# Performance work log

Measured on AMD Instinct MI355X. Metric: run time of the kernel, lower is better.

## Reference

```python
import jax, jax.numpy as jnp
import numpy as np

B, S, Lb, C, CP, H = 64, 4, 64, 32, 16, 4
LN_EPS = 1e-5


def layer_norm(x, g, b):
    mu = jnp.mean(x, axis=-1, keepdims=True)
    var = jnp.mean(jnp.square(x - mu), axis=-1, keepdims=True)
    return (x - mu) * jax.lax.rsqrt(var + LN_EPS) * g + b


def mha(x, w_in, b_in, w_out, b_out, h):
    # torch nn.MultiheadAttention, batch_first, self-attention
    Bx, L, Cx = x.shape
    d = Cx // h
    qkv = x @ w_in.T + b_in                      # (Bx, L, 3C)
    q, k, v = jnp.split(qkv, 3, axis=-1)
    sp = lambda t: t.reshape(Bx, L, h, d).transpose(0, 2, 1, 3)  # (Bx,h,L,d)
    q, k, v = sp(q), sp(k), sp(v)
    scale = 1.0 / jnp.sqrt(jnp.asarray(d, x.dtype))
    attn = jax.nn.softmax(jnp.einsum('bhid,bhjd->bhij', q, k) * scale, axis=-1)
    o = jnp.einsum('bhij,bhjd->bhid', attn, v).transpose(0, 2, 1, 3).reshape(Bx, L, Cx)
    return o @ w_out.T + b_out


def setup_inputs() -> dict:
    key = jax.random.key(0)
    ks = jax.random.split(key, 20)
    g = lambda i, shape, s=0.05: (jax.random.normal(ks[i], shape, dtype=jnp.float32) * s)
    inp = {
        'chip_ctcf': jax.random.normal(ks[0], (B, Lb), dtype=jnp.float32),
        'chip_hac':  jax.random.normal(ks[1], (B, Lb), dtype=jnp.float32),
        'chip_me1':  jax.random.normal(ks[2], (B, Lb), dtype=jnp.float32),
        'chip_me3':  jax.random.normal(ks[3], (B, Lb), dtype=jnp.float32),
        'embed_w': g(4, (C, 1)), 'embed_b': g(5, (C,)),
        'pos_embed': g(6, (1, 1, Lb, C), 0.02),
        'row_in_w': g(7, (3 * C, C)), 'row_in_b': g(8, (3 * C,)),
        'row_out_w': g(9, (C, C)), 'row_out_b': g(10, (C,)),
        'row_ln_g': jnp.ones((C,), jnp.float32), 'row_ln_b': jnp.zeros((C,), jnp.float32),
        'col_in_w': g(11, (3 * C, C)), 'col_in_b': g(12, (3 * C,)),
        'col_out_w': g(13, (C, C)), 'col_out_b': g(14, (C,)),
        'col_ln_g': jnp.ones((C,), jnp.float32), 'col_ln_b': jnp.zeros((C,), jnp.float32),
        'proj_w': g(15, (CP, C * C)), 'proj_b': g(16, (CP,)),
        'pln_g': jnp.ones((CP,), jnp.float32), 'pln_b': jnp.zeros((CP,), jnp.float32),
    }
    return inp


def reference(chip_ctcf, chip_hac, chip_me1, chip_me3,
              embed_w, embed_b, pos_embed,
              row_in_w, row_in_b, row_out_w, row_out_b, row_ln_g, row_ln_b,
              col_in_w, col_in_b, col_out_w, col_out_b, col_ln_g, col_ln_b,
              proj_w, proj_b, pln_g, pln_b):
    Bv = chip_ctcf.shape[0]
    signals = jnp.stack([chip_ctcf, chip_hac, chip_me1, chip_me3], axis=1)  # (B,4,64)
    # Linear(1, C): scalar embed
    msa = signals[..., None] * embed_w[:, 0] + embed_b                      # (B,4,64,C)
    msa = msa + pos_embed
    # row attention over the 64 bins, per track
    x = msa.reshape(Bv * S, Lb, C)
    x = layer_norm(x + mha(x, row_in_w, row_in_b, row_out_w, row_out_b, H), row_ln_g, row_ln_b)
    msa = x.reshape(Bv, S, Lb, C)
    # column attention over the 4 tracks, per bin
    x = msa.transpose(0, 2, 1, 3).reshape(Bv * Lb, S, C)
    x = layer_norm(x + mha(x, col_in_w, col_in_b, col_out_w, col_out_b, H), col_ln_g, col_ln_b)
    msa = x.reshape(Bv, Lb, S, C).transpose(0, 2, 1, 3)                     # (B,4,64,C)
    # outer product of the track-mean (as written in the torch source)
    m = jnp.mean(msa, axis=1)                                               # (B,64,C)
    pair = jnp.einsum('bic,bjd->bijcd', m, m).reshape(Bv, Lb, Lb, C * C)    # (B,64,64,1024)
    nrm = jnp.sqrt(jnp.sum(jnp.square(pair), axis=-1, keepdims=True))
    pair = pair / jnp.maximum(nrm, 1e-6)                                    # F.normalize eps=1e-6
    feat = pair @ proj_w.T + proj_b                                         # (B,64,64,CP)
    feat = layer_norm(feat, pln_g, pln_b)
    feat = feat * jax.nn.sigmoid(feat)                                      # SiLU
    return feat.transpose(0, 3, 1, 2)                                       # (B,CP,64,64)
```

## Files before the change

kernel.cpp:

```cpp
#include <hip/hip_runtime.h>

#define LN_EPS 1e-5f

__device__ __forceinline__ float dot8(float4 a0, float4 a1, float4 b0, float4 b1) {
    return a0.x * b0.x + a0.y * b0.y + a0.z * b0.z + a0.w * b0.w +
           a1.x * b1.x + a1.y * b1.y + a1.z * b1.z + a1.w * b1.w;
}

__global__ __launch_bounds__(512, 4) void k_row(
    const float* __restrict__ ctcf, const float* __restrict__ hac,
    const float* __restrict__ me1,  const float* __restrict__ me3,
    const float* __restrict__ ew,   const float* __restrict__ eb,
    const float* __restrict__ pe,
    const float* __restrict__ w_in, const float* __restrict__ b_in,
    const float* __restrict__ w_out,const float* __restrict__ b_out,
    const float* __restrict__ ln_g, const float* __restrict__ ln_b,
    float* __restrict__ msaR)
{
    __shared__ float sx[64][33];
    __shared__ float sqkv[64 * 100];
    __shared__ float so[32][33];

    const int blk = blockIdx.x;
    const int qh  = blk & 1;
    const int s   = (blk >> 1) & 3;
    const int b   = blk >> 3;
    const int qbase = qh * 32;
    const int tid = threadIdx.x;

    const float* chip = (s == 0) ? ctcf : (s == 1) ? hac : (s == 2) ? me1 : me3;

    const int l  = tid & 63;
    const int cg = __builtin_amdgcn_readfirstlane(tid >> 6);

    float xr[32];
    {
        const float cv = chip[b * 64 + l];
        const float4* pe4 = (const float4*)&pe[l * 32];
        const float4* ew4 = (const float4*)ew;
        const float4* eb4 = (const float4*)eb;
#pragma unroll
        for (int c4 = 0; c4 < 8; ++c4) {
            float4 pv = pe4[c4], e = ew4[c4], bb = eb4[c4];
            xr[c4 * 4 + 0] = cv * e.x + bb.x + pv.x;
            xr[c4 * 4 + 1] = cv * e.y + bb.y + pv.y;
            xr[c4 * 4 + 2] = cv * e.z + bb.z + pv.z;
            xr[c4 * 4 + 3] = cv * e.w + bb.w + pv.w;
        }
    }
    if (cg == 0) {
#pragma unroll
        for (int c = 0; c < 32; ++c) sx[l][c] = xr[c];
    }

#pragma unroll
    for (int i = 0; i < 12; ++i) {
        const int cc = i * 8 + cg;
        const float4* wr4 = (const float4*)&w_in[cc * 32];
        float acc = b_in[cc];
#pragma unroll
        for (int c4 = 0; c4 < 8; ++c4) {
            float4 wv = wr4[c4];
            acc += xr[c4 * 4 + 0] * wv.x + xr[c4 * 4 + 1] * wv.y +
                   xr[c4 * 4 + 2] * wv.z + xr[c4 * 4 + 3] * wv.w;
        }
        sqkv[l * 100 + cc] = acc;
    }
    __syncthreads();

    {
        const int h  = tid >> 7;
        const int q  = (tid >> 2) & 31;
        const int kc = tid & 3;
        const int lq = qbase + q;
        const float4* qp = (const float4*)&sqkv[lq * 100 + h * 8];
        float4 q0 = qp[0], q1 = qp[1];
        const float scale = 0.35355339059327373f;

        float sc[16];
#pragma unroll
        for (int jj = 0; jj < 16; ++jj) {
            const int j = kc * 16 + ((jj + kc) & 15);
            const float4* kp = (const float4*)&sqkv[j * 100 + 32 + h * 8];
            sc[jj] = dot8(q0, q1, kp[0], kp[1]) * scale;
        }
        float m0 = fmaxf(fmaxf(fmaxf(sc[0], sc[1]),  fmaxf(sc[2], sc[3])),
                         fmaxf(fmaxf(sc[4], sc[5]),  fmaxf(sc[6], sc[7])));
        float m1 = fmaxf(fmaxf(fmaxf(sc[8], sc[9]),  fmaxf(sc[10], sc[11])),
                         fmaxf(fmaxf(sc[12], sc[13]), fmaxf(sc[14], sc[15])));
        float mx = fmaxf(m0, m1);
        mx = fmaxf(mx, __shfl_xor(mx, 1, 64));
        mx = fmaxf(mx, __shfl_xor(mx, 2, 64));

        float den = 0.f, a[8];
#pragma unroll
        for (int dd = 0; dd < 8; ++dd) a[dd] = 0.f;
#pragma unroll
        for (int jj = 0; jj < 16; ++jj) {
            const int j = kc * 16 + ((jj + kc) & 15);
            float w = __expf(sc[jj] - mx);
            den += w;
            const float4* vp = (const float4*)&sqkv[j * 100 + 64 + h * 8];
            float4 v0 = vp[0], v1 = vp[1];
            a[0] += w * v0.x;  a[1] += w * v0.y;
            a[2] += w * v0.z;  a[3] += w * v0.w;
            a[4] += w * v1.x;  a[5] += w * v1.y;
            a[6] += w * v1.z;  a[7] += w * v1.w;
        }
#pragma unroll
        for (int off = 1; off <= 2; off <<= 1) {
            den += __shfl_xor(den, off, 64);
#pragma unroll
            for (int dd = 0; dd < 8; ++dd) a[dd] += __shfl_xor(a[dd], off, 64);
        }
        float inv = 1.f / den;
        float r0, r1;
        if      (kc == 0) { r0 = a[0]; r1 = a[1]; }
        else if (kc == 1) { r0 = a[2]; r1 = a[3]; }
        else if (kc == 2) { r0 = a[4]; r1 = a[5]; }
        else              { r0 = a[6]; r1 = a[7]; }
        so[q][h * 8 + kc * 2 + 0] = r0 * inv;
        so[q][h * 8 + kc * 2 + 1] = r1 * inv;
    }
    __syncthreads();

    {
        const int lq2 = tid & 31;
        const int cB  = tid >> 5;
        float orow[32];
#pragma unroll
        for (int k = 0; k < 32; ++k) orow[k] = so[lq2][k];
#pragma unroll
        for (int i = 0; i < 2; ++i) {
            int c = cB + i * 16;
            const float4* wr4 = (const float4*)&w_out[c * 32];
            float acc = b_out[c] + sx[qbase + lq2][c];
#pragma unroll
            for (int k4 = 0; k4 < 8; ++k4) {
                float4 wv = wr4[k4];
                acc += orow[k4 * 4 + 0] * wv.x + orow[k4 * 4 + 1] * wv.y +
                       orow[k4 * 4 + 2] * wv.z + orow[k4 * 4 + 3] * wv.w;
            }
            sqkv[lq2 * 100 + c] = acc;
        }
    }
    __syncthreads();

    {
        const int c = tid & 31;
#pragma unroll
        for (int p = 0; p < 2; ++p) {
            int r = p * 16 + (tid >> 5);
            float v = sqkv[r * 100 + c];
            float s1 = v;
#pragma unroll
            for (int off = 16; off >= 1; off >>= 1) s1 += __shfl_xor(s1, off, 64);
            float mu = s1 * (1.f / 32.f);
            float d = v - mu;
            float s2 = d * d;
#pragma unroll
            for (int off = 16; off >= 1; off >>= 1) s2 += __shfl_xor(s2, off, 64);
            float rstd = rsqrtf(s2 * (1.f / 32.f) + LN_EPS);
            msaR[((b * 4 + s) * 64 + qbase + r) * 32 + c] = d * rstd * ln_g[c] + ln_b[c];
        }
    }
}

__global__ __launch_bounds__(256, 4) void k_col(
    const float* __restrict__ msaR,
    const float* __restrict__ w_in, const float* __restrict__ b_in,
    const float* __restrict__ w_out,const float* __restrict__ b_out,
    const float* __restrict__ ln_g, const float* __restrict__ ln_b,
    float* __restrict__ m_out, float* __restrict__ nrm_out)
{
    __shared__ float sx[16][33];
    __shared__ float sqkv[16 * 100];
    __shared__ float so[16][33];

    const int bx = blockIdx.x;
    const int b  = bx >> 4;
    const int l0 = (bx & 15) * 4;
    const int tid = threadIdx.x;

    for (int n = tid; n < 512; n += 256) {
        int r = n >> 5, c = n & 31;
        int lo = r >> 2, s = r & 3;
        sx[r][c] = msaR[((b * 4 + s) * 64 + l0 + lo) * 32 + c];
    }
    __syncthreads();

    {
        const int rr = tid & 15;
        const int cg = tid >> 4;
        float xr[32];
#pragma unroll
        for (int c = 0; c < 32; ++c) xr[c] = sx[rr][c];
#pragma unroll
        for (int i = 0; i < 6; ++i) {
            int cc = i * 16 + cg;
            const float4* wr4 = (const float4*)&w_in[cc * 32];
            float acc = b_in[cc];
#pragma unroll
            for (int c4 = 0; c4 < 8; ++c4) {
                float4 wv = wr4[c4];
                acc += xr[c4 * 4 + 0] * wv.x + xr[c4 * 4 + 1] * wv.y +
                       xr[c4 * 4 + 2] * wv.z + xr[c4 * 4 + 3] * wv.w;
            }
            sqkv[rr * 100 + cc] = acc;
        }
    }
    __syncthreads();

    if (tid < 64) {
        const int lo = tid >> 4, h = (tid >> 2) & 3, ia = tid & 3;
        const float scale = 0.35355339059327373f;
        const float4* qp = (const float4*)&sqkv[(lo * 4 + ia) * 100 + h * 8];
        float4 q0 = qp[0], q1 = qp[1];
        float sc[4];
        float mx = -1e30f;
#pragma unroll
        for (int jj = 0; jj < 4; ++jj) {
            const float4* kp = (const float4*)&sqkv[(lo * 4 + jj) * 100 + 32 + h * 8];
            sc[jj] = dot8(q0, q1, kp[0], kp[1]) * scale;
            mx = fmaxf(mx, sc[jj]);
        }
        float den = 0.f;
#pragma unroll
        for (int jj = 0; jj < 4; ++jj) { sc[jj] = __expf(sc[jj] - mx); den += sc[jj]; }
        float inv = 1.f / den;
        float a[8];
#pragma unroll
        for (int dd = 0; dd < 8; ++dd) a[dd] = 0.f;
#pragma unroll
        for (int jj = 0; jj < 4; ++jj) {
            const float4* vp = (const float4*)&sqkv[(lo * 4 + jj) * 100 + 64 + h * 8];
            float4 v0 = vp[0], v1 = vp[1];
            float wgt = sc[jj];
            a[0] += wgt * v0.x;  a[1] += wgt * v0.y;
            a[2] += wgt * v0.z;  a[3] += wgt * v0.w;
            a[4] += wgt * v1.x;  a[5] += wgt * v1.y;
            a[6] += wgt * v1.z;  a[7] += wgt * v1.w;
        }
#pragma unroll
        for (int dd = 0; dd < 8; ++dd) so[lo * 4 + ia][h * 8 + dd] = a[dd] * inv;
    }
    __syncthreads();

    {
        const int r2 = tid & 15;
        const int cB = tid >> 4;
        float orow[32];
#pragma unroll
        for (int k = 0; k < 32; ++k) orow[k] = so[r2][k];
#pragma unroll
        for (int i = 0; i < 2; ++i) {
            int c = cB + i * 16;
            const float4* wr4 = (const float4*)&w_out[c * 32];
            float acc = b_out[c] + sx[r2][c];
#pragma unroll
            for (int k4 = 0; k4 < 8; ++k4) {
                float4 wv = wr4[k4];
                acc += orow[k4 * 4 + 0] * wv.x + orow[k4 * 4 + 1] * wv.y +
                       orow[k4 * 4 + 2] * wv.z + orow[k4 * 4 + 3] * wv.w;
            }
            sqkv[r2 * 100 + c] = acc;
        }
    }
    __syncthreads();

    {
        const int c = tid & 31;
#pragma unroll
        for (int p = 0; p < 2; ++p) {
            int r = p * 8 + (tid >> 5);
            float v = sqkv[r * 100 + c];
            float s1 = v;
#pragma unroll
            for (int off = 16; off >= 1; off >>= 1) s1 += __shfl_xor(s1, off, 64);
            float mu = s1 * (1.f / 32.f);
            float d = v - mu;
            float s2 = d * d;
#pragma unroll
            for (int off = 16; off >= 1; off >>= 1) s2 += __shfl_xor(s2, off, 64);
            float rstd = rsqrtf(s2 * (1.f / 32.f) + LN_EPS);
            so[r][c] = d * rstd;
        }
    }
    __syncthreads();

    if (tid < 128) {
        const int lo = tid >> 5, c = tid & 31;
        float mval = 0.25f * (so[lo * 4 + 0][c] + so[lo * 4 + 1][c] +
                              so[lo * 4 + 2][c] + so[lo * 4 + 3][c]) * ln_g[c] + ln_b[c];
        m_out[(b * 64 + l0 + lo) * 32 + c] = mval;
        float q2 = mval * mval;
#pragma unroll
        for (int off = 16; off >= 1; off >>= 1) q2 += __shfl_xor(q2, off, 64);
        if (c == 0) nrm_out[b * 64 + l0 + lo] = sqrtf(q2);
    }
}

__global__ __launch_bounds__(256, 4) void k_pair(
    const float* __restrict__ m, const float* __restrict__ nrm,
    const float* __restrict__ pw, const float* __restrict__ pb,
    const float* __restrict__ pg, const float* __restrict__ pbeta,
    float* __restrict__ out)
{
    __shared__ float smj[64][36];
    __shared__ float sT[4 * 520];
    __shared__ float snj[64];
    __shared__ float sbias[16], sgam[16], sbet[16];

    const int bx = blockIdx.x;
    const int b  = bx >> 4;
    const int i0 = (bx & 15) * 4;
    const int tid = threadIdx.x;
    const int lane = tid & 63, w = tid >> 6;

    const int rem0 = tid, rem1 = tid + 256;
    const float* pw0 = pw + (rem0 >> 5) * 1024 + (rem0 & 31);
    const float* pw1 = pw + (rem1 >> 5) * 1024 + (rem1 & 31);
    float w0[32], w1[32];
#pragma unroll
    for (int c = 0; c < 32; ++c) { w0[c] = pw0[c * 32]; w1[c] = pw1[c * 32]; }

    const float* mb = m + b * 2048;
    for (int n = tid; n < 2048; n += 256) smj[n >> 5][n & 31] = mb[n];
    if (tid < 64) snj[tid] = nrm[b * 64 + tid];
    if (tid < 16) {
        sbias[tid] = pb[tid];
        sgam[tid]  = pg[tid];
        sbet[tid]  = pbeta[tid];
    }
    __syncthreads();

#pragma unroll
    for (int il = 0; il < 4; ++il) {
        const float4* mr4 = (const float4*)&smj[i0 + il][0];
        float a0 = 0.f, a1 = 0.f;
#pragma unroll
        for (int c4 = 0; c4 < 8; ++c4) {
            float4 mv = mr4[c4];
            a0 += mv.x * w0[c4 * 4 + 0] + mv.y * w0[c4 * 4 + 1] +
                  mv.z * w0[c4 * 4 + 2] + mv.w * w0[c4 * 4 + 3];
            a1 += mv.x * w1[c4 * 4 + 0] + mv.y * w1[c4 * 4 + 1] +
                  mv.z * w1[c4 * 4 + 2] + mv.w * w1[c4 * 4 + 3];
        }
        sT[il * 520 + rem0] = a0;
        sT[il * 520 + rem1] = a1;
    }
    __syncthreads();

    const int j = lane;
    float mj[32];
    {
        const float4* mjp = (const float4*)&smj[j][0];
#pragma unroll
        for (int d4 = 0; d4 < 8; ++d4) {
            float4 t = mjp[d4];
            mj[d4 * 4 + 0] = t.x;  mj[d4 * 4 + 1] = t.y;
            mj[d4 * 4 + 2] = t.z;  mj[d4 * 4 + 3] = t.w;
        }
    }
    const float nj = snj[j];

    {
        const int il = w;
        const int ig = i0 + il;
        const float invn = 1.f / fmaxf(snj[ig] * nj, 1e-6f);
        float f[16];
#pragma unroll
        for (int cp = 0; cp < 16; ++cp) {
            const float4* tr = (const float4*)&sT[il * 520 + cp * 32];
            float acc = 0.f;
#pragma unroll
            for (int d4 = 0; d4 < 8; ++d4) {
                float4 tv = tr[d4];
                acc += tv.x * mj[d4 * 4 + 0] + tv.y * mj[d4 * 4 + 1] +
                       tv.z * mj[d4 * 4 + 2] + tv.w * mj[d4 * 4 + 3];
            }
            f[cp] = acc * invn + sbias[cp];
        }
        float mu = 0.f;
#pragma unroll
        for (int cp = 0; cp < 16; ++cp) mu += f[cp];
        mu *= (1.f / 16.f);
        float var = 0.f;
#pragma unroll
        for (int cp = 0; cp < 16; ++cp) { float d = f[cp] - mu; var += d * d; }
        var *= (1.f / 16.f);
        const float rstd = rsqrtf(var + LN_EPS);
#pragma unroll
        for (int cp = 0; cp < 16; ++cp) {
            float v = (f[cp] - mu) * rstd * sgam[cp] + sbet[cp];
            float sl = v / (1.f + __expf(-v));
            out[((b * 16 + cp) * 64 + ig) * 64 + j] = sl;
        }
    }
}

extern "C" void kernel_launch(void* const* d_in, const int* in_sizes, int n_in,
                              void* d_out, int out_size, void* d_ws, size_t ws_size,
                              hipStream_t stream) {
    const float* ctcf  = (const float*)d_in[0];
    const float* hac   = (const float*)d_in[1];
    const float* me1   = (const float*)d_in[2];
    const float* me3   = (const float*)d_in[3];
    const float* ew    = (const float*)d_in[4];
    const float* ebias = (const float*)d_in[5];
    const float* pe    = (const float*)d_in[6];
    const float* riw   = (const float*)d_in[7];
    const float* rib   = (const float*)d_in[8];
    const float* row_  = (const float*)d_in[9];
    const float* rob   = (const float*)d_in[10];
    const float* rlg   = (const float*)d_in[11];
    const float* rlb   = (const float*)d_in[12];
    const float* ciw   = (const float*)d_in[13];
    const float* cib   = (const float*)d_in[14];
    const float* cow   = (const float*)d_in[15];
    const float* cob   = (const float*)d_in[16];
    const float* clg   = (const float*)d_in[17];
    const float* clb   = (const float*)d_in[18];
    const float* pw    = (const float*)d_in[19];
    const float* pb    = (const float*)d_in[20];
    const float* pg    = (const float*)d_in[21];
    const float* pbt   = (const float*)d_in[22];

    float* out = (float*)d_out;

    float* msaR = (float*)d_out;
    float* mbuf = (float*)d_ws;
    float* nbuf = mbuf + 64 * 64 * 32;

    k_row<<<512, 512, 0, stream>>>(ctcf, hac, me1, me3, ew, ebias, pe,
                                   riw, rib, row_, rob, rlg, rlb, msaR);
    k_col<<<1024, 256, 0, stream>>>(msaR, ciw, cib, cow, cob, clg, clb,
                                    mbuf, nbuf);
    k_pair<<<1024, 256, 0, stream>>>(mbuf, nbuf, pw, pb, pg, pbt, out);
}
```

Baseline: 144.2 us.

## Fuse row, column and pair stages into one cooperative kernel with grid sync

Merges the three separate kernel launches into a single cooperative kernel of 512 blocks that runs the row-attention, column-attention and pair-projection stages in sequence, separated by grid-wide barriers. The aim is to remove the launch gaps and tail effects between kernels. In exchange, the column and pair stages now run on 512 blocks of 512 threads instead of 1024 blocks of 256, so their work split changes, and grid.sync adds its own cost. The old three-kernel path is kept as a fallback when occupancy is too low or the cooperative launch fails.

```diff
diff --git a/kernel.cpp b/kernel.cpp
--- a/kernel.cpp
+++ b/kernel.cpp
@@ -1,10 +1,404 @@
 #include <hip/hip_runtime.h>
+#include <hip/hip_cooperative_groups.h>
+
+namespace cg = cooperative_groups;
 
 #define LN_EPS 1e-5f
 
 __device__ __forceinline__ float dot8(float4 a0, float4 a1, float4 b0, float4 b1) {
     return a0.x * b0.x + a0.y * b0.y + a0.z * b0.z + a0.w * b0.w +
            a1.x * b1.x + a1.y * b1.y + a1.z * b1.z + a1.w * b1.w;
+}
+
+__global__ __launch_bounds__(512, 4) void k_fused(
+    const float* __restrict__ ctcf, const float* __restrict__ hac,
+    const float* __restrict__ me1,  const float* __restrict__ me3,
+    const float* __restrict__ ew,   const float* __restrict__ eb,
+    const float* __restrict__ pe,
+    const float* __restrict__ riw,  const float* __restrict__ rib,
+    const float* __restrict__ row_w,const float* __restrict__ row_b,
+    const float* __restrict__ rlg,  const float* __restrict__ rlb,
+    const float* __restrict__ ciw,  const float* __restrict__ cib,
+    const float* __restrict__ cow,  const float* __restrict__ cob,
+    const float* __restrict__ clg,  const float* __restrict__ clb,
+    const float* __restrict__ pw,   const float* __restrict__ pb,
+    const float* __restrict__ pg,   const float* __restrict__ pbt,
+    float* msaR, float* mbuf, float* nbuf, float* out)
+{
+    __shared__ float smem[7552];
+    const int bx  = blockIdx.x;
+    const int tid = threadIdx.x;
+    cg::grid_group grid = cg::this_grid();
+
+    {
+        float* sqkv = smem;
+        float* so   = smem + 6400;
+
+        const int qh = bx & 1, s = (bx >> 1) & 3, b = bx >> 3;
+        const int qbase = qh * 32;
+        const float* chip = (s == 0) ? ctcf : (s == 1) ? hac : (s == 2) ? me1 : me3;
+        const int l   = tid & 63;
+        const int cgi = __builtin_amdgcn_readfirstlane(tid >> 6);
+
+        float xr[32];
+        {
+            const float cv = chip[b * 64 + l];
+            const float4* pe4 = (const float4*)&pe[l * 32];
+            const float4* ew4 = (const float4*)ew;
+            const float4* eb4 = (const float4*)eb;
+#pragma unroll
+            for (int c4 = 0; c4 < 8; ++c4) {
+                float4 pv = pe4[c4], e = ew4[c4], bb = eb4[c4];
+                xr[c4 * 4 + 0] = cv * e.x + bb.x + pv.x;
+                xr[c4 * 4 + 1] = cv * e.y + bb.y + pv.y;
+                xr[c4 * 4 + 2] = cv * e.z + bb.z + pv.z;
+                xr[c4 * 4 + 3] = cv * e.w + bb.w + pv.w;
+            }
+        }
+
+        {
+            const int cc0 = cgi * 12;
+            float acc[12];
+#pragma unroll
+            for (int ii = 0; ii < 12; ++ii) acc[ii] = rib[cc0 + ii];
+#pragma unroll
+            for (int ii = 0; ii < 12; ++ii) {
+                const float4* wr4 = (const float4*)&riw[(cc0 + ii) * 32];
+#pragma unroll
+                for (int c4 = 0; c4 < 8; ++c4) {
+                    float4 wv = wr4[c4];
+                    acc[ii] += xr[c4 * 4 + 0] * wv.x + xr[c4 * 4 + 1] * wv.y +
+                               xr[c4 * 4 + 2] * wv.z + xr[c4 * 4 + 3] * wv.w;
+                }
+            }
+            float* dst = &sqkv[l * 100 + cc0];
+            *(float4*)(dst + 0) = make_float4(acc[0], acc[1], acc[2],  acc[3]);
+            *(float4*)(dst + 4) = make_float4(acc[4], acc[5], acc[6],  acc[7]);
+            *(float4*)(dst + 8) = make_float4(acc[8], acc[9], acc[10], acc[11]);
+        }
+        __syncthreads();
+
+        {
+            const int h  = tid >> 7;
+            const int q  = (tid >> 2) & 31;
+            const int kc = tid & 3;
+            const int lq = qbase + q;
+            const float4* qp = (const float4*)&sqkv[lq * 100 + h * 8];
+            float4 q0 = qp[0], q1 = qp[1];
+            const float scale = 0.35355339059327373f;
+
+            float sc[16];
+#pragma unroll
+            for (int jj = 0; jj < 16; ++jj) {
+                const int j = kc * 16 + ((jj + kc) & 15);
+                const float4* kp = (const float4*)&sqkv[j * 100 + 32 + h * 8];
+                sc[jj] = dot8(q0, q1, kp[0], kp[1]) * scale;
+            }
+            float m0 = fmaxf(fmaxf(fmaxf(sc[0], sc[1]),  fmaxf(sc[2], sc[3])),
+                             fmaxf(fmaxf(sc[4], sc[5]),  fmaxf(sc[6], sc[7])));
+            float m1 = fmaxf(fmaxf(fmaxf(sc[8], sc[9]),  fmaxf(sc[10], sc[11])),
+                             fmaxf(fmaxf(sc[12], sc[13]), fmaxf(sc[14], sc[15])));
+            float mx = fmaxf(m0, m1);
+            mx = fmaxf(mx, __shfl_xor(mx, 1, 64));
+            mx = fmaxf(mx, __shfl_xor(mx, 2, 64));
+
+            float den = 0.f, a[8];
+#pragma unroll
+            for (int dd = 0; dd < 8; ++dd) a[dd] = 0.f;
+#pragma unroll
+            for (int jj = 0; jj < 16; ++jj) {
+                const int j = kc * 16 + ((jj + kc) & 15);
+                float wgt = __expf(sc[jj] - mx);
+                den += wgt;
+                const float4* vp = (const float4*)&sqkv[j * 100 + 64 + h * 8];
+                float4 v0 = vp[0], v1 = vp[1];
+                a[0] += wgt * v0.x;  a[1] += wgt * v0.y;
+                a[2] += wgt * v0.z;  a[3] += wgt * v0.w;
+                a[4] += wgt * v1.x;  a[5] += wgt * v1.y;
+                a[6] += wgt * v1.z;  a[7] += wgt * v1.w;
+            }
+#pragma unroll
+            for (int off = 1; off <= 2; off <<= 1) {
+                den += __shfl_xor(den, off, 64);
+#pragma unroll
+                for (int dd = 0; dd < 8; ++dd) a[dd] += __shfl_xor(a[dd], off, 64);
+            }
+            float inv = 1.f / den;
+            float r0, r1;
+            if      (kc == 0) { r0 = a[0]; r1 = a[1]; }
+            else if (kc == 1) { r0 = a[2]; r1 = a[3]; }
+            else if (kc == 2) { r0 = a[4]; r1 = a[5]; }
+            else              { r0 = a[6]; r1 = a[7]; }
+            so[q * 36 + h * 8 + kc * 2 + 0] = r0 * inv;
+            so[q * 36 + h * 8 + kc * 2 + 1] = r1 * inv;
+        }
+        __syncthreads();
+
+        {
+            const int lq2 = tid & 31;
+            const int cB  = tid >> 5;
+            const int lg  = qbase + lq2;
+            const float cvr = chip[b * 64 + lg];
+            float orow[32];
+            const float4* sop = (const float4*)&so[lq2 * 36];
+#pragma unroll
+            for (int k4 = 0; k4 < 8; ++k4) {
+                float4 t = sop[k4];
+                orow[k4 * 4 + 0] = t.x;  orow[k4 * 4 + 1] = t.y;
+                orow[k4 * 4 + 2] = t.z;  orow[k4 * 4 + 3] = t.w;
+            }
+#pragma unroll
+            for (int i = 0; i < 2; ++i) {
+                int c = cB + i * 16;
+                const float4* wr4 = (const float4*)&row_w[c * 32];
+                float acc = row_b[c] + (cvr * ew[c] + eb[c] + pe[lg * 32 + c]);
+#pragma unroll
+                for (int k4 = 0; k4 < 8; ++k4) {
+                    float4 wv = wr4[k4];
+                    acc += orow[k4 * 4 + 0] * wv.x + orow[k4 * 4 + 1] * wv.y +
+                           orow[k4 * 4 + 2] * wv.z + orow[k4 * 4 + 3] * wv.w;
+                }
+                sqkv[lq2 * 100 + c] = acc;
+            }
+        }
+        __syncthreads();
+
+        {
+            const int c = tid & 31;
+#pragma unroll
+            for (int p = 0; p < 2; ++p) {
+                int r = p * 16 + (tid >> 5);
+                float v = sqkv[r * 100 + c];
+                float s1 = v;
+#pragma unroll
+                for (int off = 16; off >= 1; off >>= 1) s1 += __shfl_xor(s1, off, 64);
+                float mu = s1 * (1.f / 32.f);
+                float d = v - mu;
+                float s2 = d * d;
+#pragma unroll
+                for (int off = 16; off >= 1; off >>= 1) s2 += __shfl_xor(s2, off, 64);
+                float rstd = rsqrtf(s2 * (1.f / 32.f) + LN_EPS);
+                msaR[((b * 4 + s) * 64 + qbase + r) * 32 + c] =
+                    d * rstd * rlg[c] + rlb[c];
+            }
+        }
+    }
+    grid.sync();
+
+    {
+        float* sx2   = smem;
+        float* sqkv2 = smem + 1056;
+        float* so2   = smem + 4256;
+
+        const int b  = bx >> 3;
+        const int l0 = (bx & 7) * 8;
+
+        for (int n = tid; n < 1024; n += 512) {
+            int r = n >> 5, c = n & 31;
+            int lo = r >> 2, s = r & 3;
+            sx2[r * 33 + c] = msaR[((b * 4 + s) * 64 + l0 + lo) * 32 + c];
+        }
+        __syncthreads();
+
+        {
+            const int rr = tid & 31;
+            const int cg2 = tid >> 5;
+            float xr[32];
+#pragma unroll
+            for (int c = 0; c < 32; ++c) xr[c] = sx2[rr * 33 + c];
+#pragma unroll
+            for (int i = 0; i < 6; ++i) {
+                int cc = i * 16 + cg2;
+                const float4* wr4 = (const float4*)&ciw[cc * 32];
+                float acc = cib[cc];
+#pragma unroll
+                for (int c4 = 0; c4 < 8; ++c4) {
+                    float4 wv = wr4[c4];
+                    acc += xr[c4 * 4 + 0] * wv.x + xr[c4 * 4 + 1] * wv.y +
+                           xr[c4 * 4 + 2] * wv.z + xr[c4 * 4 + 3] * wv.w;
+                }
+                sqkv2[rr * 100 + cc] = acc;
+            }
+        }
+        __syncthreads();
+
+        if (tid < 128) {
+            const int lo = tid >> 4, h = (tid >> 2) & 3, ia = tid & 3;
+            const float scale = 0.35355339059327373f;
+            const float4* qp = (const float4*)&sqkv2[(lo * 4 + ia) * 100 + h * 8];
+            float4 q0 = qp[0], q1 = qp[1];
+            float sc[4];
+            float mx = -1e30f;
+#pragma unroll
+            for (int jj = 0; jj < 4; ++jj) {
+                const float4* kp = (const float4*)&sqkv2[(lo * 4 + jj) * 100 + 32 + h * 8];
+                sc[jj] = dot8(q0, q1, kp[0], kp[1]) * scale;
+                mx = fmaxf(mx, sc[jj]);
+            }
+            float den = 0.f;
+#pragma unroll
+            for (int jj = 0; jj < 4; ++jj) { sc[jj] = __expf(sc[jj] - mx); den += sc[jj]; }
+            float inv = 1.f / den;
+            float a[8];
+#pragma unroll
+            for (int dd = 0; dd < 8; ++dd) a[dd] = 0.f;
+#pragma unroll
+            for (int jj = 0; jj < 4; ++jj) {
+                const float4* vp = (const float4*)&sqkv2[(lo * 4 + jj) * 100 + 64 + h * 8];
+                float4 v0 = vp[0], v1 = vp[1];
+                float wgt = sc[jj];
+                a[0] += wgt * v0.x;  a[1] += wgt * v0.y;
+                a[2] += wgt * v0.z;  a[3] += wgt * v0.w;
+                a[4] += wgt * v1.x;  a[5] += wgt * v1.y;
+                a[6] += wgt * v1.z;  a[7] += wgt * v1.w;
+            }
+#pragma unroll
+            for (int dd = 0; dd < 8; ++dd) so2[(lo * 4 + ia) * 36 + h * 8 + dd] = a[dd] * inv;
+        }
+        __syncthreads();
+
+        {
+            const int r2 = tid & 31;
+            const int cB = tid >> 5;
+            float orow[32];
+            const float4* sop = (const float4*)&so2[r2 * 36];
+#pragma unroll
+            for (int k4 = 0; k4 < 8; ++k4) {
+                float4 t = sop[k4];
+                orow[k4 * 4 + 0] = t.x;  orow[k4 * 4 + 1] = t.y;
+                orow[k4 * 4 + 2] = t.z;  orow[k4 * 4 + 3] = t.w;
+            }
+#pragma unroll
+            for (int i = 0; i < 2; ++i) {
+                int c = cB + i * 16;
+                const float4* wr4 = (const float4*)&cow[c * 32];
+                float acc = cob[c] + sx2[r2 * 33 + c];
+#pragma unroll
+                for (int k4 = 0; k4 < 8; ++k4) {
+                    float4 wv = wr4[k4];
+                    acc += orow[k4 * 4 + 0] * wv.x + orow[k4 * 4 + 1] * wv.y +
+                           orow[k4 * 4 + 2] * wv.z + orow[k4 * 4 + 3] * wv.w;
+                }
+                sqkv2[r2 * 100 + c] = acc;
+            }
+        }
+        __syncthreads();
+
+        {
+            const int c = tid & 31;
+#pragma unroll
+            for (int p = 0; p < 2; ++p) {
+                int r = p * 16 + (tid >> 5);
+                float v = sqkv2[r * 100 + c];
+                float s1 = v;
+#pragma unroll
+                for (int off = 16; off >= 1; off >>= 1) s1 += __shfl_xor(s1, off, 64);
+                float mu = s1 * (1.f / 32.f);
+                float d = v - mu;
+                float s2 = d * d;
+#pragma unroll
+                for (int off = 16; off >= 1; off >>= 1) s2 += __shfl_xor(s2, off, 64);
+                float rstd = rsqrtf(s2 * (1.f / 32.f) + LN_EPS);
+                so2[r * 36 + c] = d * rstd;
+            }
+        }
+        __syncthreads();
+
+        if (tid < 256) {
+            const int lo = tid >> 5, c = tid & 31;
+            float mval = 0.25f * (so2[(lo * 4 + 0) * 36 + c] + so2[(lo * 4 + 1) * 36 + c] +
+                                  so2[(lo * 4 + 2) * 36 + c] + so2[(lo * 4 + 3) * 36 + c]) *
+                         clg[c] + clb[c];
+            mbuf[(b * 64 + l0 + lo) * 32 + c] = mval;
+            float q2 = mval * mval;
+#pragma unroll
+            for (int off = 16; off >= 1; off >>= 1) q2 += __shfl_xor(q2, off, 64);
+            if (c == 0) nbuf[b * 64 + l0 + lo] = sqrtf(q2);
+        }
+    }
+    grid.sync();
+
+    {
+        float* smj = smem;
+        float* sT  = smem + 2304;
+        float* snj = smem + 6464;
+        float* sb  = smem + 6528;
+        float* sg  = smem + 6544;
+        float* sbt = smem + 6560;
+
+        const int b  = bx >> 3;
+        const int i0 = (bx & 7) * 8;
+        const int lane = tid & 63, w = tid >> 6;
+
+        const float* pwp = pw + (tid >> 5) * 1024 + (tid & 31);
+        float w0[32];
+#pragma unroll
+        for (int c = 0; c < 32; ++c) w0[c] = pwp[c * 32];
+
+        const float* mb = mbuf + b * 2048;
+        for (int n = tid; n < 2048; n += 512) smj[(n >> 5) * 36 + (n & 31)] = mb[n];
+        if (tid < 64) snj[tid] = nbuf[b * 64 + tid];
+        if (tid < 16) { sb[tid] = pb[tid]; sg[tid] = pg[tid]; sbt[tid] = pbt[tid]; }
+        __syncthreads();
+
+#pragma unroll
+        for (int il = 0; il < 8; ++il) {
+            const float4* mr4 = (const float4*)&smj[(i0 + il) * 36];
+            float a0 = 0.f;
+#pragma unroll
+            for (int c4 = 0; c4 < 8; ++c4) {
+                float4 mv = mr4[c4];
+                a0 += mv.x * w0[c4 * 4 + 0] + mv.y * w0[c4 * 4 + 1] +
+                      mv.z * w0[c4 * 4 + 2] + mv.w * w0[c4 * 4 + 3];
+            }
+            sT[il * 520 + tid] = a0;
+        }
+        __syncthreads();
+
+        const int j = lane;
+        float mj[32];
+        {
+            const float4* mjp = (const float4*)&smj[j * 36];
+#pragma unroll
+            for (int d4 = 0; d4 < 8; ++d4) {
+                float4 t = mjp[d4];
+                mj[d4 * 4 + 0] = t.x;  mj[d4 * 4 + 1] = t.y;
+                mj[d4 * 4 + 2] = t.z;  mj[d4 * 4 + 3] = t.w;
+            }
+        }
+        const float nj = snj[j];
+        const int il = w;
+        const int ig = i0 + il;
+        const float invn = 1.f / fmaxf(snj[ig] * nj, 1e-6f);
+        float f[16];
+#pragma unroll
+        for (int cp = 0; cp < 16; ++cp) {
+            const float4* tr = (const float4*)&sT[il * 520 + cp * 32];
+            float acc = 0.f;
+#pragma unroll
+            for (int d4 = 0; d4 < 8; ++d4) {
+                float4 tv = tr[d4];
+                acc += tv.x * mj[d4 * 4 + 0] + tv.y * mj[d4 * 4 + 1] +
+                       tv.z * mj[d4 * 4 + 2] + tv.w * mj[d4 * 4 + 3];
+            }
+            f[cp] = acc * invn + sb[cp];
+        }
+        float mu = 0.f;
+#pragma unroll
+        for (int cp = 0; cp < 16; ++cp) mu += f[cp];
+        mu *= (1.f / 16.f);
+        float var = 0.f;
+#pragma unroll
+        for (int cp = 0; cp < 16; ++cp) { float d = f[cp] - mu; var += d * d; }
+        var *= (1.f / 16.f);
+        const float rstd = rsqrtf(var + LN_EPS);
+#pragma unroll
+        for (int cp = 0; cp < 16; ++cp) {
+            float v = (f[cp] - mu) * rstd * sg[cp] + sbt[cp];
+            float sl = v / (1.f + __expf(-v));
+            out[((b * 16 + cp) * 64 + ig) * 64 + j] = sl;
+        }
+    }
 }
 
 __global__ __launch_bounds__(512, 4) void k_row(
@@ -426,15 +820,40 @@
     const float* pg    = (const float*)d_in[21];
     const float* pbt   = (const float*)d_in[22];
 
-    float* out = (float*)d_out;
+    float* outp = (float*)d_out;
 
     float* msaR = (float*)d_out;
     float* mbuf = (float*)d_ws;
     float* nbuf = mbuf + 64 * 64 * 32;
 
-    k_row<<<512, 512, 0, stream>>>(ctcf, hac, me1, me3, ew, ebias, pe,
-                                   riw, rib, row_, rob, rlg, rlb, msaR);
-    k_col<<<1024, 256, 0, stream>>>(msaR, ciw, cib, cow, cob, clg, clb,
-                                    mbuf, nbuf);
-    k_pair<<<1024, 256, 0, stream>>>(mbuf, nbuf, pw, pb, pg, pbt, out);
+    static int s_coop = -1;
+    if (s_coop < 0) {
+        int nb = 0;
+        hipError_t e = hipOccupancyMaxActiveBlocksPerMultiprocessor(
+            &nb, k_fused, 512, 0);
+        s_coop = (e == hipSuccess && nb >= 2) ? 1 : 0;
+    }
+
+    if (s_coop) {
+        void* args[] = {
+            (void*)&ctcf, (void*)&hac, (void*)&me1, (void*)&me3,
+            (void*)&ew,   (void*)&ebias, (void*)&pe,
+            (void*)&riw,  (void*)&rib, (void*)&row_, (void*)&rob,
+            (void*)&rlg,  (void*)&rlb,
+            (void*)&ciw,  (void*)&cib, (void*)&cow, (void*)&cob,
+            (void*)&clg,  (void*)&clb,
+            (void*)&pw,   (void*)&pb,  (void*)&pg,  (void*)&pbt,
+            (void*)&msaR, (void*)&mbuf, (void*)&nbuf, (void*)&outp
+        };
+        hipError_t le = hipLaunchCooperativeKernel((void*)k_fused, dim3(512),
+                                                   dim3(512), args, 0, stream);
+        if (le != hipSuccess) s_coop = 0;
+    }
+    if (!s_coop) {
+        k_row<<<512, 512, 0, stream>>>(ctcf, hac, me1, me3, ew, ebias, pe,
+                                       riw, rib, row_, rob, rlg, rlb, msaR);
+        k_col<<<1024, 256, 0, stream>>>(msaR, ciw, cib, cow, cob, clg, clb,
+                                        mbuf, nbuf);
+        k_pair<<<1024, 256, 0, stream>>>(mbuf, nbuf, pw, pb, pg, pbt, outp);
+    }
 }
```

Measured after the change: 144.8 us. No clear change (+0.4%).

## Split row attention into QKV and attention kernels, shrink per-block work

Applied to the files above, without the earlier changes.

Splits the fused row-attention kernel into a QKV projection kernel that writes QKV to a scratch area in the output buffer, and an attention kernel that handles 8 queries per block with K/V staged in shared memory. The column kernel now processes 2 bins per block with one thread per output element. The goal is more blocks and higher occupancy (256 threads, 8 blocks per CU) in place of large 512-thread blocks. The cost is an extra launch, a global round-trip for QKV, and K/V being reloaded by each of the 8 query blocks.

```diff
diff --git a/kernel.cpp b/kernel.cpp
--- a/kernel.cpp
+++ b/kernel.cpp
@@ -7,220 +7,219 @@
            a1.x * b1.x + a1.y * b1.y + a1.z * b1.z + a1.w * b1.w;
 }
 
-__global__ __launch_bounds__(512, 4) void k_row(
+__global__ __launch_bounds__(256, 8) void k_qkv1(
     const float* __restrict__ ctcf, const float* __restrict__ hac,
     const float* __restrict__ me1,  const float* __restrict__ me3,
     const float* __restrict__ ew,   const float* __restrict__ eb,
     const float* __restrict__ pe,
-    const float* __restrict__ w_in, const float* __restrict__ b_in,
-    const float* __restrict__ w_out,const float* __restrict__ b_out,
-    const float* __restrict__ ln_g, const float* __restrict__ ln_b,
+    const float* __restrict__ riw,  const float* __restrict__ rib,
+    float* __restrict__ qkvR)
+{
+    const int bx   = blockIdx.x;
+    const int slab = bx >> 8;
+    const int bs   = bx & 255;
+    const int s    = bs & 3, b = bs >> 2;
+    const int tid  = threadIdx.x;
+    const int r    = tid >> 2;
+    const int cc0  = slab * 16 + (tid & 3) * 4;
+
+    const float* chip = (s == 0) ? ctcf : (s == 1) ? hac : (s == 2) ? me1 : me3;
+    const float cv = chip[b * 64 + r];
+
+    const float4* ew4 = (const float4*)ew;
+    const float4* eb4 = (const float4*)eb;
+    const float4* pe4 = (const float4*)&pe[r * 32];
+    const float4* w0  = (const float4*)&riw[(cc0 + 0) * 32];
+    const float4* w1  = (const float4*)&riw[(cc0 + 1) * 32];
+    const float4* w2  = (const float4*)&riw[(cc0 + 2) * 32];
+    const float4* w3  = (const float4*)&riw[(cc0 + 3) * 32];
+
+    float a0 = rib[cc0 + 0], a1 = rib[cc0 + 1], a2 = rib[cc0 + 2], a3 = rib[cc0 + 3];
+#pragma unroll
+    for (int c4 = 0; c4 < 8; ++c4) {
+        float4 e = ew4[c4], bb = eb4[c4], pv = pe4[c4];
+        float x0 = cv * e.x + bb.x + pv.x;
+        float x1 = cv * e.y + bb.y + pv.y;
+        float x2 = cv * e.z + bb.z + pv.z;
+        float x3 = cv * e.w + bb.w + pv.w;
+        float4 v0 = w0[c4], v1 = w1[c4], v2 = w2[c4], v3 = w3[c4];
+        a0 += x0 * v0.x + x1 * v0.y + x2 * v0.z + x3 * v0.w;
+        a1 += x0 * v1.x + x1 * v1.y + x2 * v1.z + x3 * v1.w;
+        a2 += x0 * v2.x + x1 * v2.y + x2 * v2.z + x3 * v2.w;
+        a3 += x0 * v3.x + x1 * v3.y + x2 * v3.z + x3 * v3.w;
+    }
+    *(float4*)&qkvR[bs * 6144 + r * 96 + cc0] = make_float4(a0, a1, a2, a3);
+}
+
+__global__ __launch_bounds__(256, 8) void k_attn1(
+    const float* __restrict__ ctcf, const float* __restrict__ hac,
+    const float* __restrict__ me1,  const float* __restrict__ me3,
+    const float* __restrict__ ew,   const float* __restrict__ eb,
+    const float* __restrict__ pe,
+    const float* __restrict__ qkvR,
+    const float* __restrict__ row_w,const float* __restrict__ row_b,
+    const float* __restrict__ rlg,  const float* __restrict__ rlb,
     float* __restrict__ msaR)
 {
-    __shared__ float sx[64][33];
-    __shared__ float sqkv[64 * 100];
-    __shared__ float so[32][33];
-
-    const int blk = blockIdx.x;
-    const int qh  = blk & 1;
-    const int s   = (blk >> 1) & 3;
-    const int b   = blk >> 3;
-    const int qbase = qh * 32;
+    __shared__ float kv[64][68];
+    __shared__ float so[8][36];
+
+    const int bx = blockIdx.x;
+    const int bs = bx >> 3;
+    const int q0 = (bx & 7) * 8;
+    const int s  = bs & 3, b = bs >> 2;
     const int tid = threadIdx.x;
 
-    const float* chip = (s == 0) ? ctcf : (s == 1) ? hac : (s == 2) ? me1 : me3;
-
-    const int l  = tid & 63;
-    const int cg = __builtin_amdgcn_readfirstlane(tid >> 6);
-
-    float xr[32];
-    {
-        const float cv = chip[b * 64 + l];
-        const float4* pe4 = (const float4*)&pe[l * 32];
-        const float4* ew4 = (const float4*)ew;
-        const float4* eb4 = (const float4*)eb;
-#pragma unroll
-        for (int c4 = 0; c4 < 8; ++c4) {
-            float4 pv = pe4[c4], e = ew4[c4], bb = eb4[c4];
-            xr[c4 * 4 + 0] = cv * e.x + bb.x + pv.x;
-            xr[c4 * 4 + 1] = cv * e.y + bb.y + pv.y;
-            xr[c4 * 4 + 2] = cv * e.z + bb.z + pv.z;
-            xr[c4 * 4 + 3] = cv * e.w + bb.w + pv.w;
-        }
-    }
-    if (cg == 0) {
-#pragma unroll
-        for (int c = 0; c < 32; ++c) sx[l][c] = xr[c];
-    }
-
-#pragma unroll
-    for (int i = 0; i < 12; ++i) {
-        const int cc = i * 8 + cg;
-        const float4* wr4 = (const float4*)&w_in[cc * 32];
-        float acc = b_in[cc];
-#pragma unroll
-        for (int c4 = 0; c4 < 8; ++c4) {
-            float4 wv = wr4[c4];
-            acc += xr[c4 * 4 + 0] * wv.x + xr[c4 * 4 + 1] * wv.y +
-                   xr[c4 * 4 + 2] * wv.z + xr[c4 * 4 + 3] * wv.w;
-        }
-        sqkv[l * 100 + cc] = acc;
-    }
-    __syncthreads();
-
-    {
-        const int h  = tid >> 7;
-        const int q  = (tid >> 2) & 31;
-        const int kc = tid & 3;
-        const int lq = qbase + q;
-        const float4* qp = (const float4*)&sqkv[lq * 100 + h * 8];
-        float4 q0 = qp[0], q1 = qp[1];
+    {
+        const float* src = qkvR + bs * 6144;
+#pragma unroll
+        for (int k = 0; k < 4; ++k) {
+            int idx  = tid + k * 256;
+            int row  = idx >> 4;
+            int part = idx & 15;
+            *(float4*)&kv[row][part * 4] =
+                *(const float4*)&src[row * 96 + 32 + part * 4];
+        }
+    }
+    __syncthreads();
+
+    {
+        const int h  = tid >> 6;
+        const int q8 = (tid >> 3) & 7;
+        const int kc = tid & 7;
+        const int lq = q0 + q8;
+        const float4* qp = (const float4*)&qkvR[bs * 6144 + lq * 96 + h * 8];
+        float4 qv0 = qp[0], qv1 = qp[1];
         const float scale = 0.35355339059327373f;
 
-        float sc[16];
-#pragma unroll
-        for (int jj = 0; jj < 16; ++jj) {
-            const int j = kc * 16 + ((jj + kc) & 15);
-            const float4* kp = (const float4*)&sqkv[j * 100 + 32 + h * 8];
-            sc[jj] = dot8(q0, q1, kp[0], kp[1]) * scale;
-        }
-        float m0 = fmaxf(fmaxf(fmaxf(sc[0], sc[1]),  fmaxf(sc[2], sc[3])),
-                         fmaxf(fmaxf(sc[4], sc[5]),  fmaxf(sc[6], sc[7])));
-        float m1 = fmaxf(fmaxf(fmaxf(sc[8], sc[9]),  fmaxf(sc[10], sc[11])),
-                         fmaxf(fmaxf(sc[12], sc[13]), fmaxf(sc[14], sc[15])));
-        float mx = fmaxf(m0, m1);
+        float sc[8];
+#pragma unroll
+        for (int jj = 0; jj < 8; ++jj) {
+            const int j = kc * 8 + ((jj + kc) & 7);
+            const float4* kp = (const float4*)&kv[j][h * 8];
+            sc[jj] = dot8(qv0, qv1, kp[0], kp[1]) * scale;
+        }
+        float mx = fmaxf(fmaxf(fmaxf(sc[0], sc[1]), fmaxf(sc[2], sc[3])),
+                         fmaxf(fmaxf(sc[4], sc[5]), fmaxf(sc[6], sc[7])));
         mx = fmaxf(mx, __shfl_xor(mx, 1, 64));
         mx = fmaxf(mx, __shfl_xor(mx, 2, 64));
+        mx = fmaxf(mx, __shfl_xor(mx, 4, 64));
 
         float den = 0.f, a[8];
 #pragma unroll
         for (int dd = 0; dd < 8; ++dd) a[dd] = 0.f;
 #pragma unroll
-        for (int jj = 0; jj < 16; ++jj) {
-            const int j = kc * 16 + ((jj + kc) & 15);
-            float w = __expf(sc[jj] - mx);
-            den += w;
-            const float4* vp = (const float4*)&sqkv[j * 100 + 64 + h * 8];
+        for (int jj = 0; jj < 8; ++jj) {
+            const int j = kc * 8 + ((jj + kc) & 7);
+            float wgt = __expf(sc[jj] - mx);
+            den += wgt;
+            const float4* vp = (const float4*)&kv[j][32 + h * 8];
             float4 v0 = vp[0], v1 = vp[1];
-            a[0] += w * v0.x;  a[1] += w * v0.y;
-            a[2] += w * v0.z;  a[3] += w * v0.w;
-            a[4] += w * v1.x;  a[5] += w * v1.y;
-            a[6] += w * v1.z;  a[7] += w * v1.w;
-        }
-#pragma unroll
-        for (int off = 1; off <= 2; off <<= 1) {
+            a[0] += wgt * v0.x;  a[1] += wgt * v0.y;
+            a[2] += wgt * v0.z;  a[3] += wgt * v0.w;
+            a[4] += wgt * v1.x;  a[5] += wgt * v1.y;
+            a[6] += wgt * v1.z;  a[7] += wgt * v1.w;
+        }
+#pragma unroll
+        for (int off = 1; off <= 4; off <<= 1) {
             den += __shfl_xor(den, off, 64);
 #pragma unroll
             for (int dd = 0; dd < 8; ++dd) a[dd] += __shfl_xor(a[dd], off, 64);
         }
         float inv = 1.f / den;
-        float r0, r1;
-        if      (kc == 0) { r0 = a[0]; r1 = a[1]; }
-        else if (kc == 1) { r0 = a[2]; r1 = a[3]; }
-        else if (kc == 2) { r0 = a[4]; r1 = a[5]; }
-        else              { r0 = a[6]; r1 = a[7]; }
-        so[q][h * 8 + kc * 2 + 0] = r0 * inv;
-        so[q][h * 8 + kc * 2 + 1] = r1 * inv;
-    }
-    __syncthreads();
-
-    {
-        const int lq2 = tid & 31;
-        const int cB  = tid >> 5;
-        float orow[32];
-#pragma unroll
-        for (int k = 0; k < 32; ++k) orow[k] = so[lq2][k];
-#pragma unroll
-        for (int i = 0; i < 2; ++i) {
-            int c = cB + i * 16;
-            const float4* wr4 = (const float4*)&w_out[c * 32];
-            float acc = b_out[c] + sx[qbase + lq2][c];
-#pragma unroll
-            for (int k4 = 0; k4 < 8; ++k4) {
-                float4 wv = wr4[k4];
-                acc += orow[k4 * 4 + 0] * wv.x + orow[k4 * 4 + 1] * wv.y +
-                       orow[k4 * 4 + 2] * wv.z + orow[k4 * 4 + 3] * wv.w;
-            }
-            sqkv[lq2 * 100 + c] = acc;
-        }
-    }
-    __syncthreads();
-
-    {
-        const int c = tid & 31;
-#pragma unroll
-        for (int p = 0; p < 2; ++p) {
-            int r = p * 16 + (tid >> 5);
-            float v = sqkv[r * 100 + c];
-            float s1 = v;
-#pragma unroll
-            for (int off = 16; off >= 1; off >>= 1) s1 += __shfl_xor(s1, off, 64);
-            float mu = s1 * (1.f / 32.f);
-            float d = v - mu;
-            float s2 = d * d;
-#pragma unroll
-            for (int off = 16; off >= 1; off >>= 1) s2 += __shfl_xor(s2, off, 64);
-            float rstd = rsqrtf(s2 * (1.f / 32.f) + LN_EPS);
-            msaR[((b * 4 + s) * 64 + qbase + r) * 32 + c] = d * rstd * ln_g[c] + ln_b[c];
-        }
-    }
-}
-
-__global__ __launch_bounds__(256, 4) void k_col(
+        float rv = a[0];
+        if (kc == 1) rv = a[1];
+        else if (kc == 2) rv = a[2];
+        else if (kc == 3) rv = a[3];
+        else if (kc == 4) rv = a[4];
+        else if (kc == 5) rv = a[5];
+        else if (kc == 6) rv = a[6];
+        else if (kc == 7) rv = a[7];
+        so[q8][h * 8 + kc] = rv * inv;
+    }
+    __syncthreads();
+
+    {
+        const int r  = tid >> 5;
+        const int c  = tid & 31;
+        const int lq = q0 + r;
+        const float* chip = (s == 0) ? ctcf : (s == 1) ? hac : (s == 2) ? me1 : me3;
+        const float cv = chip[b * 64 + lq];
+
+        const float4* sop = (const float4*)&so[r][0];
+        const float4* wr4 = (const float4*)&row_w[c * 32];
+        float acc = row_b[c] + (cv * ew[c] + eb[c] + pe[lq * 32 + c]);
+#pragma unroll
+        for (int k4 = 0; k4 < 8; ++k4) {
+            float4 ov = sop[k4], wv = wr4[k4];
+            acc += ov.x * wv.x + ov.y * wv.y + ov.z * wv.z + ov.w * wv.w;
+        }
+        float s1 = acc;
+#pragma unroll
+        for (int off = 16; off >= 1; off >>= 1) s1 += __shfl_xor(s1, off, 64);
+        float mu = s1 * (1.f / 32.f);
+        float d = acc - mu;
+        float s2 = d * d;
+#pragma unroll
+        for (int off = 16; off >= 1; off >>= 1) s2 += __shfl_xor(s2, off, 64);
+        float rstd = rsqrtf(s2 * (1.f / 32.f) + LN_EPS);
+        msaR[(bs * 64 + lq) * 32 + c] = d * rstd * rlg[c] + rlb[c];
+    }
+}
+
+__global__ __launch_bounds__(256, 8) void k_colfused(
     const float* __restrict__ msaR,
-    const float* __restrict__ w_in, const float* __restrict__ b_in,
-    const float* __restrict__ w_out,const float* __restrict__ b_out,
-    const float* __restrict__ ln_g, const float* __restrict__ ln_b,
+    const float* __restrict__ ciw,  const float* __restrict__ cib,
+    const float* __restrict__ cow,  const float* __restrict__ cob,
+    const float* __restrict__ clg,  const float* __restrict__ clb,
     float* __restrict__ m_out, float* __restrict__ nrm_out)
 {
-    __shared__ float sx[16][33];
-    __shared__ float sqkv[16 * 100];
-    __shared__ float so[16][33];
+    __shared__ float sx[8][36];
+    __shared__ float sq[8][100];
+    __shared__ float so[8][36];
+    __shared__ float pr[8][36];
 
     const int bx = blockIdx.x;
-    const int b  = bx >> 4;
-    const int l0 = (bx & 15) * 4;
+    const int b  = bx >> 5;
+    const int l0 = (bx & 31) * 2;
     const int tid = threadIdx.x;
-
-    for (int n = tid; n < 512; n += 256) {
-        int r = n >> 5, c = n & 31;
+    const int r  = tid >> 5;
+    const int c  = tid & 31;
+
+    {
         int lo = r >> 2, s = r & 3;
         sx[r][c] = msaR[((b * 4 + s) * 64 + l0 + lo) * 32 + c];
     }
     __syncthreads();
 
     {
-        const int rr = tid & 15;
-        const int cg = tid >> 4;
-        float xr[32];
-#pragma unroll
-        for (int c = 0; c < 32; ++c) xr[c] = sx[rr][c];
-#pragma unroll
-        for (int i = 0; i < 6; ++i) {
-            int cc = i * 16 + cg;
-            const float4* wr4 = (const float4*)&w_in[cc * 32];
-            float acc = b_in[cc];
-#pragma unroll
-            for (int c4 = 0; c4 < 8; ++c4) {
-                float4 wv = wr4[c4];
-                acc += xr[c4 * 4 + 0] * wv.x + xr[c4 * 4 + 1] * wv.y +
-                       xr[c4 * 4 + 2] * wv.z + xr[c4 * 4 + 3] * wv.w;
-            }
-            sqkv[rr * 100 + cc] = acc;
-        }
-    }
-    __syncthreads();
-
-    if (tid < 64) {
-        const int lo = tid >> 4, h = (tid >> 2) & 3, ia = tid & 3;
+        const float4* xr4 = (const float4*)&sx[r][0];
+        const float4* wq  = (const float4*)&ciw[c * 32];
+        const float4* wk  = (const float4*)&ciw[(32 + c) * 32];
+        const float4* wv  = (const float4*)&ciw[(64 + c) * 32];
+        float aq = cib[c], ak = cib[32 + c], av = cib[64 + c];
+#pragma unroll
+        for (int k4 = 0; k4 < 8; ++k4) {
+            float4 xv = xr4[k4];
+            float4 q = wq[k4], k = wk[k4], v = wv[k4];
+            aq += xv.x * q.x + xv.y * q.y + xv.z * q.z + xv.w * q.w;
+            ak += xv.x * k.x + xv.y * k.y + xv.z * k.z + xv.w * k.w;
+            av += xv.x * v.x + xv.y * v.y + xv.z * v.z + xv.w * v.w;
+        }
+        sq[r][c] = aq; sq[r][32 + c] = ak; sq[r][64 + c] = av;
+    }
+    __syncthreads();
+
+    if (tid < 32) {
+        const int lo = tid >> 4, ia = (tid >> 2) & 3, h = tid & 3;
         const float scale = 0.35355339059327373f;
-        const float4* qp = (const float4*)&sqkv[(lo * 4 + ia) * 100 + h * 8];
+        const float4* qp = (const float4*)&sq[lo * 4 + ia][h * 8];
         float4 q0 = qp[0], q1 = qp[1];
         float sc[4];
         float mx = -1e30f;
 #pragma unroll
         for (int jj = 0; jj < 4; ++jj) {
-            const float4* kp = (const float4*)&sqkv[(lo * 4 + jj) * 100 + 32 + h * 8];
+            const float4* kp = (const float4*)&sq[lo * 4 + jj][32 + h * 8];
             sc[jj] = dot8(q0, q1, kp[0], kp[1]) * scale;
             mx = fmaxf(mx, sc[jj]);
         }
@@ -233,7 +232,7 @@
         for (int dd = 0; dd < 8; ++dd) a[dd] = 0.f;
 #pragma unroll
         for (int jj = 0; jj < 4; ++jj) {
-            const float4* vp = (const float4*)&sqkv[(lo * 4 + jj) * 100 + 64 + h * 8];
+            const float4* vp = (const float4*)&sq[lo * 4 + jj][64 + h * 8];
             float4 v0 = vp[0], v1 = vp[1];
             float wgt = sc[jj];
             a[0] += wgt * v0.x;  a[1] += wgt * v0.y;
@@ -247,56 +246,37 @@
     __syncthreads();
 
     {
-        const int r2 = tid & 15;
-        const int cB = tid >> 4;
-        float orow[32];
-#pragma unroll
-        for (int k = 0; k < 32; ++k) orow[k] = so[r2][k];
-#pragma unroll
-        for (int i = 0; i < 2; ++i) {
-            int c = cB + i * 16;
-            const float4* wr4 = (const float4*)&w_out[c * 32];
-            float acc = b_out[c] + sx[r2][c];
-#pragma unroll
-            for (int k4 = 0; k4 < 8; ++k4) {
-                float4 wv = wr4[k4];
-                acc += orow[k4 * 4 + 0] * wv.x + orow[k4 * 4 + 1] * wv.y +
-                       orow[k4 * 4 + 2] * wv.z + orow[k4 * 4 + 3] * wv.w;
-            }
-            sqkv[r2 * 100 + c] = acc;
-        }
-    }
-    __syncthreads();
-
-    {
-        const int c = tid & 31;
-#pragma unroll
-        for (int p = 0; p < 2; ++p) {
-            int r = p * 8 + (tid >> 5);
-            float v = sqkv[r * 100 + c];
-            float s1 = v;
-#pragma unroll
-            for (int off = 16; off >= 1; off >>= 1) s1 += __shfl_xor(s1, off, 64);
-            float mu = s1 * (1.f / 32.f);
-            float d = v - mu;
-            float s2 = d * d;
-#pragma unroll
-            for (int off = 16; off >= 1; off >>= 1) s2 += __shfl_xor(s2, off, 64);
-            float rstd = rsqrtf(s2 * (1.f / 32.f) + LN_EPS);
-            so[r][c] = d * rstd;
-        }
-    }
-    __syncthreads();
-
-    if (tid < 128) {
-        const int lo = tid >> 5, c = tid & 31;
-        float mval = 0.25f * (so[lo * 4 + 0][c] + so[lo * 4 + 1][c] +
-                              so[lo * 4 + 2][c] + so[lo * 4 + 3][c]) * ln_g[c] + ln_b[c];
-        m_out[(b * 64 + l0 + lo) * 32 + c] = mval;
+        const float4* sop = (const float4*)&so[r][0];
+        const float4* wr4 = (const float4*)&cow[c * 32];
+        float acc = cob[c] + sx[r][c];
+#pragma unroll
+        for (int k4 = 0; k4 < 8; ++k4) {
+            float4 ov = sop[k4], wv = wr4[k4];
+            acc += ov.x * wv.x + ov.y * wv.y + ov.z * wv.z + ov.w * wv.w;
+        }
+        float s1 = acc;
+#pragma unroll
+        for (int off = 16; off >= 1; off >>= 1) s1 += __shfl_xor(s1, off, 64);
+        float mu = s1 * (1.f / 32.f);
+        float d = acc - mu;
+        float s2 = d * d;
+#pragma unroll
+        for (int off = 16; off >= 1; off >>= 1) s2 += __shfl_xor(s2, off, 64);
+        float rstd = rsqrtf(s2 * (1.f / 32.f) + LN_EPS);
+        pr[r][c] = d * rstd;
+    }
+    __syncthreads();
+
+    if (tid < 64) {
+        const int lo = tid >> 5, cc = tid & 31;
+        float mval = 0.25f * (pr[lo * 4 + 0][cc] + pr[lo * 4 + 1][cc] +
+                              pr[lo * 4 + 2][cc] + pr[lo * 4 + 3][cc]) *
+                     clg[cc] + clb[cc];
+        m_out[(b * 64 + l0 + lo) * 32 + cc] = mval;
         float q2 = mval * mval;
 #pragma unroll
         for (int off = 16; off >= 1; off >>= 1) q2 += __shfl_xor(q2, off, 64);
-        if (c == 0) nrm_out[b * 64 + l0 + lo] = sqrtf(q2);
+        if (cc == 0) nrm_out[b * 64 + l0 + lo] = sqrtf(q2);
     }
 }
 
@@ -426,15 +406,18 @@
     const float* pg    = (const float*)d_in[21];
     const float* pbt   = (const float*)d_in[22];
 
-    float* out = (float*)d_out;
+    float* outp = (float*)d_out;
 
     float* msaR = (float*)d_out;
+    float* qkvR = msaR + 524288;
     float* mbuf = (float*)d_ws;
     float* nbuf = mbuf + 64 * 64 * 32;
 
-    k_row<<<512, 512, 0, stream>>>(ctcf, hac, me1, me3, ew, ebias, pe,
-                                   riw, rib, row_, rob, rlg, rlb, msaR);
-    k_col<<<1024, 256, 0, stream>>>(msaR, ciw, cib, cow, cob, clg, clb,
-                                    mbuf, nbuf);
-    k_pair<<<1024, 256, 0, stream>>>(mbuf, nbuf, pw, pb, pg, pbt, out);
-}
+    k_qkv1<<<1536, 256, 0, stream>>>(ctcf, hac, me1, me3, ew, ebias, pe,
+                                     riw, rib, qkvR);
+    k_attn1<<<2048, 256, 0, stream>>>(ctcf, hac, me1, me3, ew, ebias, pe,
+                                      qkvR, row_, rob, rlg, rlb, msaR);
+    k_colfused<<<2048, 256, 0, stream>>>(msaR, ciw, cib, cow, cob, clg, clb,
+                                         mbuf, nbuf);
+    k_pair<<<1024, 256, 0, stream>>>(mbuf, nbuf, pw, pb, pg, pbt, outp);
+}
```

Result: slower. 204.3 us (+41.7%).
